# Performance work log

Measured on AMD Instinct MI355X. Metric: run time of the kernel, lower is better.

Reference implementation:

```python
import jax, jax.numpy as jnp
import numpy as np

N_NODES = 50000
N_EDGES = 1_600_000
IN_DIM, HID_DIM, OUT_DIM = 128, 128, 64


def setup_inputs() -> dict:
    key = jax.random.key(0)
    k_x, k_e, k_w1, k_b1, k_w2, k_b2 = jax.random.split(key, 6)
    x = jax.random.normal(k_x, (N_NODES, IN_DIM), dtype=jnp.float32)
    edge_index = jax.random.randint(k_e, (2, N_EDGES), 0, N_NODES)
    # Learned params (PyG GCNConv: linear weight + bias per layer)
    W1 = jax.random.normal(k_w1, (IN_DIM, HID_DIM), dtype=jnp.float32) * (1.0 / np.sqrt(IN_DIM))
    b1 = jax.random.normal(k_b1, (HID_DIM,), dtype=jnp.float32) * 0.02
    W2 = jax.random.normal(k_w2, (HID_DIM, OUT_DIM), dtype=jnp.float32) * (1.0 / np.sqrt(HID_DIM))
    b2 = jax.random.normal(k_b2, (OUT_DIM,), dtype=jnp.float32) * 0.02
    return {"x": x, "edge_index": edge_index, "W1": W1, "b1": b1, "W2": W2, "b2": b2}


def _gcn_conv(x, W, b, src, dst, norm, n):
    # x: [N, d_in]; transform first (d small), then gather-scale-scatter over edges.
    xw = x @ W                                   # [N, d_out]
    msg = xw[src] * norm[:, None]                # [E+N, d_out] gathered messages
    out = jax.ops.segment_sum(msg, dst, num_segments=n)
    return out + b


def reference(x, edge_index, W1, b1, W2, b2):
    n = x.shape[0]
    # GCN normalization with self-loops: A_hat = D^-1/2 (A + I) D^-1/2
    loop = jnp.arange(n, dtype=edge_index.dtype)
    src = jnp.concatenate([edge_index[0], loop])
    dst = jnp.concatenate([edge_index[1], loop])
    deg = jnp.zeros((n,), x.dtype).at[dst].add(1.0)
    dinv = jnp.where(deg > 0, jax.lax.rsqrt(deg), 0.0)
    norm = dinv[src] * dinv[dst]                 # [E+N]
    h = _gcn_conv(x, W1, b1, src, dst, norm, n)
    h = jax.nn.relu(h)
    # F.dropout(training=self.training): eval mode -> identity
    out = _gcn_conv(h, W2, b2, src, dst, norm, n)
    return out
```

## Files before the change

### kernel.cpp

```cpp
#include <hip/hip_runtime.h>
#include <cstddef>

#define MAXB 512
#define BSHIFT 7
#define ACHUNK 8192

__device__ inline unsigned pack_bf16x2(float a, float b) {
    unsigned ua = __float_as_uint(a), ub = __float_as_uint(b);
    ua = (ua + 0x7FFFu + ((ua >> 16) & 1u)) >> 16;
    ub = (ub + 0x7FFFu + ((ub >> 16) & 1u)) >> 16;
    return ua | (ub << 16);
}
__device__ inline float bf_lo(unsigned u) { return __uint_as_float(u << 16); }
__device__ inline float bf_hi(unsigned u) { return __uint_as_float(u & 0xFFFF0000u); }

__global__ __launch_bounds__(512) void k_zero512(int* __restrict__ p) {
    p[threadIdx.x] = 0;
}

__global__ __launch_bounds__(256) void k_histA(const int* __restrict__ dst, int* __restrict__ bcnt,
                                               int E, int nbuck) {
    __shared__ int hist[MAXB];
    const int tid = threadIdx.x;
    const int e0  = blockIdx.x * ACHUNK;
    const int e1  = min(e0 + ACHUNK, E);
    for (int i = tid; i < nbuck; i += 256) hist[i] = 0;
    __syncthreads();
    for (int e = e0 + tid; e < e1; e += 256)
        atomicAdd(&hist[dst[e] >> BSHIFT], 1);
    __syncthreads();
    for (int i = tid; i < nbuck; i += 256)
        if (hist[i]) atomicAdd(&bcnt[i], hist[i]);
}

__global__ __launch_bounds__(512) void k_bscan(const int* __restrict__ bcnt, int* __restrict__ bstart,
                                               int* __restrict__ bcur) {
    __shared__ int sh[512];
    const int t = threadIdx.x;
    int v = bcnt[t];
    sh[t] = v;
    __syncthreads();
    for (int d = 1; d < 512; d <<= 1) {
        int u = (t >= d) ? sh[t - d] : 0;
        __syncthreads();
        sh[t] += u;
        __syncthreads();
    }
    int ex = sh[t] - v;
    bstart[t] = ex;
    bcur[t]   = ex;
}

__global__ __launch_bounds__(256) void k_passA(const int* __restrict__ src, const int* __restrict__ dst,
                                               int* __restrict__ bcur, int2* __restrict__ tmp,
                                               int E, int nbuck) {
    __shared__ int hist[MAXB];
    __shared__ int gbase[MAXB];
    const int tid = threadIdx.x;
    const int e0  = blockIdx.x * ACHUNK;
    const int e1  = min(e0 + ACHUNK, E);
    for (int i = tid; i < nbuck; i += 256) hist[i] = 0;
    __syncthreads();
    for (int e = e0 + tid; e < e1; e += 256)
        atomicAdd(&hist[dst[e] >> BSHIFT], 1);
    __syncthreads();
    for (int i = tid; i < nbuck; i += 256) {
        int c = hist[i];
        gbase[i] = c ? atomicAdd(&bcur[i], c) : 0;
        hist[i] = 0;
    }
    __syncthreads();
    for (int e = e0 + tid; e < e1; e += 256) {
        int d = dst[e];
        int b = d >> BSHIFT;
        int slot = atomicAdd(&hist[b], 1);
        tmp[gbase[b] + slot] = make_int2(src[e], d);
    }
}

__global__ __launch_bounds__(256) void k_passB(const int2* __restrict__ tmp, const int* __restrict__ bstart,
                                               const int* __restrict__ bcnt, int* __restrict__ deg,
                                               float* __restrict__ dinv, int* __restrict__ off,
                                               int* __restrict__ esrc, int N) {
    __shared__ int cnt[1 << BSHIFT];
    __shared__ int loff[1 << BSHIFT];
    __shared__ int cur[1 << BSHIFT];
    const int b     = blockIdx.x;
    const int tid   = threadIdx.x;
    const int node0 = b << BSHIFT;
    const int base  = bstart[b];
    const int cntB  = bcnt[b];

    if (tid < 128) cnt[tid] = 0;
    __syncthreads();
    for (int i = tid; i < cntB; i += 256)
        atomicAdd(&cnt[tmp[base + i].y - node0], 1);
    __syncthreads();
    if (tid < 128) loff[tid] = cnt[tid];
    __syncthreads();
    for (int d = 1; d < 128; d <<= 1) {
        int u = (tid >= d && tid < 128) ? loff[tid - d] : 0;
        __syncthreads();
        if (tid < 128) loff[tid] += u;
        __syncthreads();
    }
    if (tid < 128) {
        int c  = cnt[tid];
        int ex = loff[tid] - c;
        cur[tid] = ex;
        if (node0 + tid < N) {
            deg [node0 + tid] = c + 1;
            dinv[node0 + tid] = rsqrtf((float)(c + 1));
            off [node0 + tid] = base + ex;
        }
    }
    __syncthreads();
    for (int i = tid; i < cntB; i += 256) {
        int2 ent = tmp[base + i];
        int  pos = atomicAdd(&cur[ent.y - node0], 1);
        esrc[base + pos] = ent.x;
    }
}

__global__ __launch_bounds__(256) void k_gemm1(const float* __restrict__ x, const float* __restrict__ W,
                                               unsigned* __restrict__ xwb, int M) {
    __shared__ float ws[128 * 128];
    __shared__ float xs[128][32];
    const int tid  = threadIdx.x;
    const int row0 = blockIdx.x * 32;

    for (int i = tid * 4; i < 128 * 128; i += 1024)
        *(float4*)&ws[i] = *(const float4*)&W[i];

    for (int i = tid; i < 32 * 32; i += 256) {
        int r  = i >> 5;
        int cc = (i & 31) << 2;
        float4 v = make_float4(0.f, 0.f, 0.f, 0.f);
        if (row0 + r < M) v = *(const float4*)&x[(size_t)(row0 + r) * 128 + cc];
        xs[cc + 0][r] = v.x; xs[cc + 1][r] = v.y; xs[cc + 2][r] = v.z; xs[cc + 3][r] = v.w;
    }
    __syncthreads();

    const int c0 = (tid & 31) << 2;
    const int r0 = (tid >> 5) << 2;
    float4 a0 = {0,0,0,0}, a1 = {0,0,0,0}, a2 = {0,0,0,0}, a3 = {0,0,0,0};
#pragma unroll 8
    for (int k = 0; k < 128; ++k) {
        float4 wv = *(const float4*)&ws[k * 128 + c0];
        float4 xv = *(const float4*)&xs[k][r0];
        a0.x += xv.x * wv.x; a0.y += xv.x * wv.y; a0.z += xv.x * wv.z; a0.w += xv.x * wv.w;
        a1.x += xv.y * wv.x; a1.y += xv.y * wv.y; a1.z += xv.y * wv.z; a1.w += xv.y * wv.w;
        a2.x += xv.z * wv.x; a2.y += xv.z * wv.y; a2.z += xv.z * wv.z; a2.w += xv.z * wv.w;
        a3.x += xv.w * wv.x; a3.y += xv.w * wv.y; a3.z += xv.w * wv.z; a3.w += xv.w * wv.w;
    }
    uint2* o = (uint2*)xwb;
    if (row0 + r0 + 0 < M) o[(size_t)(row0 + r0 + 0) * 32 + (c0 >> 2)] = make_uint2(pack_bf16x2(a0.x, a0.y), pack_bf16x2(a0.z, a0.w));
    if (row0 + r0 + 1 < M) o[(size_t)(row0 + r0 + 1) * 32 + (c0 >> 2)] = make_uint2(pack_bf16x2(a1.x, a1.y), pack_bf16x2(a1.z, a1.w));
    if (row0 + r0 + 2 < M) o[(size_t)(row0 + r0 + 2) * 32 + (c0 >> 2)] = make_uint2(pack_bf16x2(a2.x, a2.y), pack_bf16x2(a2.z, a2.w));
    if (row0 + r0 + 3 < M) o[(size_t)(row0 + r0 + 3) * 32 + (c0 >> 2)] = make_uint2(pack_bf16x2(a3.x, a3.y), pack_bf16x2(a3.z, a3.w));
}

__global__ __launch_bounds__(256) void k_gemm2(const float* __restrict__ h_in, const float* __restrict__ W,
                                               unsigned* __restrict__ hwb, int M) {
    __shared__ float ws[128 * 64];
    __shared__ float xs[128][32];
    const int tid  = threadIdx.x;
    const int row0 = blockIdx.x * 32;

    for (int i = tid * 4; i < 128 * 64; i += 1024)
        *(float4*)&ws[i] = *(const float4*)&W[i];

    for (int i = tid; i < 32 * 32; i += 256) {
        int r  = i >> 5;
        int cc = (i & 31) << 2;
        float4 v = make_float4(0.f, 0.f, 0.f, 0.f);
        if (row0 + r < M) {
            v = *(const float4*)&h_in[(size_t)(row0 + r) * 128 + cc];
            v.x = fmaxf(v.x, 0.f); v.y = fmaxf(v.y, 0.f);
            v.z = fmaxf(v.z, 0.f); v.w = fmaxf(v.w, 0.f);
        }
        xs[cc + 0][r] = v.x; xs[cc + 1][r] = v.y; xs[cc + 2][r] = v.z; xs[cc + 3][r] = v.w;
    }
    __syncthreads();

    const int c0 = (tid & 15) << 2;
    const int r0 = (tid >> 4) << 1;
    float4 a0 = {0,0,0,0}, a1 = {0,0,0,0};
#pragma unroll 8
    for (int k = 0; k < 128; ++k) {
        float4 wv = *(const float4*)&ws[k * 64 + c0];
        float2 xv = *(const float2*)&xs[k][r0];
        a0.x += xv.x * wv.x; a0.y += xv.x * wv.y; a0.z += xv.x * wv.z; a0.w += xv.x * wv.w;
        a1.x += xv.y * wv.x; a1.y += xv.y * wv.y; a1.z += xv.y * wv.z; a1.w += xv.y * wv.w;
    }
    uint2* o = (uint2*)hwb;
    if (row0 + r0 + 0 < M) o[(size_t)(row0 + r0 + 0) * 16 + (c0 >> 2)] = make_uint2(pack_bf16x2(a0.x, a0.y), pack_bf16x2(a0.z, a0.w));
    if (row0 + r0 + 1 < M) o[(size_t)(row0 + r0 + 1) * 16 + (c0 >> 2)] = make_uint2(pack_bf16x2(a1.x, a1.y), pack_bf16x2(a1.z, a1.w));
}

__global__ __launch_bounds__(256) void k_agg1(const uint2* __restrict__ xwb, const int* __restrict__ esrc,
                                              const int* __restrict__ off, const int* __restrict__ deg,
                                              const float* __restrict__ dinv, const float* __restrict__ b,
                                              float* __restrict__ out1, int N) {
    const int node = blockIdx.x * 4 + (threadIdx.x >> 6);
    if (node >= N) return;
    const int lane = threadIdx.x & 63;
    const int half = lane >> 5;
    const int lc   = lane & 31;
    const int c0   = lc << 2;

    const float di = dinv[node];
    float4 acc0 = {0,0,0,0}, acc1 = {0,0,0,0}, acc2 = {0,0,0,0}, acc3 = {0,0,0,0};
    if (half == 0) {
        float w0 = di * di;
        uint2  sv = xwb[(size_t)node * 32 + lc];
        float4 bb = *(const float4*)&b[c0];
        acc0.x = bb.x + bf_lo(sv.x) * w0; acc0.y = bb.y + bf_hi(sv.x) * w0;
        acc0.z = bb.z + bf_lo(sv.y) * w0; acc0.w = bb.w + bf_hi(sv.y) * w0;
    }

    const int base = off[node];
    const int cnt  = deg[node] - 1;
    for (int p0 = 0; p0 < cnt; p0 += 64) {
        int   es = 0;
        float ew = 0.f;
        if (p0 + lane < cnt) {
            es = esrc[base + p0 + lane];
            ew = dinv[es] * di;
        }
        const int take = min(64, cnt - p0);
        int j = 0;
        for (; j + 8 <= take; j += 8) {
            int i0 = j + half, i1 = j + 2 + half, i2 = j + 4 + half, i3 = j + 6 + half;
            int   s0 = __shfl(es, i0); float w0f = __shfl(ew, i0);
            int   s1 = __shfl(es, i1); float w1f = __shfl(ew, i1);
            int   s2 = __shfl(es, i2); float w2f = __shfl(ew, i2);
            int   s3 = __shfl(es, i3); float w3f = __shfl(ew, i3);
            uint2 v0 = xwb[(size_t)s0 * 32 + lc];
            uint2 v1 = xwb[(size_t)s1 * 32 + lc];
            uint2 v2 = xwb[(size_t)s2 * 32 + lc];
            uint2 v3 = xwb[(size_t)s3 * 32 + lc];
            acc0.x += bf_lo(v0.x) * w0f; acc0.y += bf_hi(v0.x) * w0f;
            acc0.z += bf_lo(v0.y) * w0f; acc0.w += bf_hi(v0.y) * w0f;
            acc1.x += bf_lo(v1.x) * w1f; acc1.y += bf_hi(v1.x) * w1f;
            acc1.z += bf_lo(v1.y) * w1f; acc1.w += bf_hi(v1.y) * w1f;
            acc2.x += bf_lo(v2.x) * w2f; acc2.y += bf_hi(v2.x) * w2f;
            acc2.z += bf_lo(v2.y) * w2f; acc2.w += bf_hi(v2.y) * w2f;
            acc3.x += bf_lo(v3.x) * w3f; acc3.y += bf_hi(v3.x) * w3f;
            acc3.z += bf_lo(v3.y) * w3f; acc3.w += bf_hi(v3.y) * w3f;
        }
        for (; j < take; j += 2) {
            int i0 = j + half;
            int   s0 = __shfl(es, i0); float w0f = __shfl(ew, i0);
            uint2 v0 = xwb[(size_t)s0 * 32 + lc];
            acc0.x += bf_lo(v0.x) * w0f; acc0.y += bf_hi(v0.x) * w0f;
            acc0.z += bf_lo(v0.y) * w0f; acc0.w += bf_hi(v0.y) * w0f;
        }
    }
    acc0.x += acc1.x + acc2.x + acc3.x;
    acc0.y += acc1.y + acc2.y + acc3.y;
    acc0.z += acc1.z + acc2.z + acc3.z;
    acc0.w += acc1.w + acc2.w + acc3.w;
    acc0.x += __shfl_xor(acc0.x, 32);
    acc0.y += __shfl_xor(acc0.y, 32);
    acc0.z += __shfl_xor(acc0.z, 32);
    acc0.w += __shfl_xor(acc0.w, 32);
    if (half == 0) *(float4*)&out1[(size_t)node * 128 + c0] = acc0;
}

__global__ __launch_bounds__(256) void k_agg2(const uint2* __restrict__ hwb, const int* __restrict__ esrc,
                                              const int* __restrict__ off, const int* __restrict__ deg,
                                              const float* __restrict__ dinv, const float* __restrict__ b,
                                              float* __restrict__ out, int N) {
    const int node = blockIdx.x * 4 + (threadIdx.x >> 6);
    if (node >= N) return;
    const int lane = threadIdx.x & 63;
    const int grp  = lane >> 4;
    const int lc   = lane & 15;
    const int c0   = lc << 2;

    const float di = dinv[node];
    float4 acc0 = {0,0,0,0}, acc1 = {0,0,0,0}, acc2 = {0,0,0,0}, acc3 = {0,0,0,0};
    if (grp == 0) {
        float w0 = di * di;
        uint2  sv = hwb[(size_t)node * 16 + lc];
        float4 bb = *(const float4*)&b[c0];
        acc0.x = bb.x + bf_lo(sv.x) * w0; acc0.y = bb.y + bf_hi(sv.x) * w0;
        acc0.z = bb.z + bf_lo(sv.y) * w0; acc0.w = bb.w + bf_hi(sv.y) * w0;
    }

    const int base = off[node];
    const int cnt  = deg[node] - 1;
    for (int p0 = 0; p0 < cnt; p0 += 64) {
        int   es = 0;
        float ew = 0.f;
        if (p0 + lane < cnt) {
            es = esrc[base + p0 + lane];
            ew = dinv[es] * di;
        }
        const int take = min(64, cnt - p0);
        int j = 0;
        for (; j + 16 <= take; j += 16) {
            int i0 = j + grp, i1 = j + 4 + grp, i2 = j + 8 + grp, i3 = j + 12 + grp;
            int   s0 = __shfl(es, i0); float w0f = __shfl(ew, i0);
            int   s1 = __shfl(es, i1); float w1f = __shfl(ew, i1);
            int   s2 = __shfl(es, i2); float w2f = __shfl(ew, i2);
            int   s3 = __shfl(es, i3); float w3f = __shfl(ew, i3);
            uint2 v0 = hwb[(size_t)s0 * 16 + lc];
            uint2 v1 = hwb[(size_t)s1 * 16 + lc];
            uint2 v2 = hwb[(size_t)s2 * 16 + lc];
            uint2 v3 = hwb[(size_t)s3 * 16 + lc];
            acc0.x += bf_lo(v0.x) * w0f; acc0.y += bf_hi(v0.x) * w0f;
            acc0.z += bf_lo(v0.y) * w0f; acc0.w += bf_hi(v0.y) * w0f;
            acc1.x += bf_lo(v1.x) * w1f; acc1.y += bf_hi(v1.x) * w1f;
            acc1.z += bf_lo(v1.y) * w1f; acc1.w += bf_hi(v1.y) * w1f;
            acc2.x += bf_lo(v2.x) * w2f; acc2.y += bf_hi(v2.x) * w2f;
            acc2.z += bf_lo(v2.y) * w2f; acc2.w += bf_hi(v2.y) * w2f;
            acc3.x += bf_lo(v3.x) * w3f; acc3.y += bf_hi(v3.x) * w3f;
            acc3.z += bf_lo(v3.y) * w3f; acc3.w += bf_hi(v3.y) * w3f;
        }
        for (; j < take; j += 4) {
            int i0 = j + grp;
            int   s0 = __shfl(es, i0); float w0f = __shfl(ew, i0);
            uint2 v0 = hwb[(size_t)s0 * 16 + lc];
            acc0.x += bf_lo(v0.x) * w0f; acc0.y += bf_hi(v0.x) * w0f;
            acc0.z += bf_lo(v0.y) * w0f; acc0.w += bf_hi(v0.y) * w0f;
        }
    }
    acc0.x += acc1.x + acc2.x + acc3.x;
    acc0.y += acc1.y + acc2.y + acc3.y;
    acc0.z += acc1.z + acc2.z + acc3.z;
    acc0.w += acc1.w + acc2.w + acc3.w;
    acc0.x += __shfl_xor(acc0.x, 16); acc0.y += __shfl_xor(acc0.y, 16);
    acc0.z += __shfl_xor(acc0.z, 16); acc0.w += __shfl_xor(acc0.w, 16);
    acc0.x += __shfl_xor(acc0.x, 32); acc0.y += __shfl_xor(acc0.y, 32);
    acc0.z += __shfl_xor(acc0.z, 32); acc0.w += __shfl_xor(acc0.w, 32);
    if (lane < 16) *(float4*)&out[(size_t)node * 64 + c0] = acc0;
}

extern "C" void kernel_launch(void* const* d_in, const int* in_sizes, int n_in,
                              void* d_out, int out_size, void* d_ws, size_t ws_size,
                              hipStream_t stream) {
    const float* x  = (const float*)d_in[0];
    const int*   ei = (const int*)  d_in[1];
    const float* W1 = (const float*)d_in[2];
    const float* b1 = (const float*)d_in[3];
    const float* W2 = (const float*)d_in[4];
    const float* b2 = (const float*)d_in[5];
    float* out = (float*)d_out;

    const int N = in_sizes[0] / 128;
    const int E = in_sizes[1] / 2;
    const int* src = ei;
    const int* dst = ei + E;
    const int NBUCK = (N + 127) / 128;
    const int NA    = (E + ACHUNK - 1) / ACHUNK;

    char* w = (char*)d_ws;
    int*      deg     = (int*)w;              w += (size_t)N * 4;
    float*    dinv    = (float*)w;            w += (size_t)N * 4;
    int*      off     = (int*)w;              w += (size_t)N * 4;
    int*      bstart  = (int*)w;              w += 512 * 4;
    int*      bcnt    = (int*)w;              w += 512 * 4;
    int*      bcur    = (int*)w;              w += 512 * 4;
    int*      esrc    = (int*)w;              w += (size_t)E * 4;
    unsigned* xwb     = (unsigned*)w;         w += (size_t)N * 128 * 2;
    float*    out1    = (float*)w;            w += (size_t)N * 128 * 4;
    unsigned* hwb     = (unsigned*)w;
    int2*     tmp     = (int2*)out1;

    k_zero512 <<<1, 512, 0, stream>>>(bcnt);
    k_histA   <<<NA, 256, 0, stream>>>(dst, bcnt, E, NBUCK);
    k_bscan   <<<1, 512, 0, stream>>>(bcnt, bstart, bcur);
    k_passA   <<<NA, 256, 0, stream>>>(src, dst, bcur, tmp, E, NBUCK);
    k_passB   <<<NBUCK, 256, 0, stream>>>(tmp, bstart, bcnt, deg, dinv, off, esrc, N);

    k_gemm1 <<<(N + 31) / 32, 256, 0, stream>>>(x, W1, xwb, N);
    k_agg1  <<<(N + 3) / 4, 256, 0, stream>>>((const uint2*)xwb, esrc, off, deg, dinv, b1, out1, N);

    k_gemm2 <<<(N + 31) / 32, 256, 0, stream>>>(out1, W2, hwb, N);
    k_agg2  <<<(N + 3) / 4, 256, 0, stream>>>((const uint2*)hwb, esrc, off, deg, dinv, b2, out, N);
}
```

Before: 248.7 us.

## Bin edges by source chunk and process 8 nodes per wave for gather locality

```diff
diff --git a/kernel.cpp b/kernel.cpp
--- a/kernel.cpp
+++ b/kernel.cpp
@@ -4,6 +4,9 @@
 #define MAXB 512
 #define BSHIFT 7
 #define ACHUNK 8192
+#define CSHIFT 13
+#define NCH 7
+#define NPW 8
 
 __device__ inline unsigned pack_bf16x2(float a, float b) {
     unsigned ua = __float_as_uint(a), ub = __float_as_uint(b);
@@ -79,24 +82,34 @@
 }
 
 __global__ __launch_bounds__(256) void k_passB(const int2* __restrict__ tmp, const int* __restrict__ bstart,
-                                               const int* __restrict__ bcnt, int* __restrict__ deg,
-                                               float* __restrict__ dinv, int* __restrict__ off,
-                                               int* __restrict__ esrc, int N) {
-    __shared__ int cnt[1 << BSHIFT];
-    __shared__ int loff[1 << BSHIFT];
-    __shared__ int cur[1 << BSHIFT];
+                                               const int* __restrict__ bcnt, float* __restrict__ dinv,
+                                               int* __restrict__ coff, int* __restrict__ esrc, int N) {
+    __shared__ int cnt2[128 * NCH];
+    __shared__ int cur2[128 * NCH];
+    __shared__ int tot[128];
+    __shared__ int loff[128];
     const int b     = blockIdx.x;
     const int tid   = threadIdx.x;
     const int node0 = b << BSHIFT;
     const int base  = bstart[b];
     const int cntB  = bcnt[b];
 
-    if (tid < 128) cnt[tid] = 0;
-    __syncthreads();
-    for (int i = tid; i < cntB; i += 256)
-        atomicAdd(&cnt[tmp[base + i].y - node0], 1);
-    __syncthreads();
-    if (tid < 128) loff[tid] = cnt[tid];
+    for (int i = tid; i < 128 * NCH; i += 256) cnt2[i] = 0;
+    __syncthreads();
+    for (int i = tid; i < cntB; i += 256) {
+        int2 ent = tmp[base + i];
+        int  nl  = ent.y - node0;
+        int  c   = min(ent.x >> CSHIFT, NCH - 1);
+        atomicAdd(&cnt2[nl * NCH + c], 1);
+    }
+    __syncthreads();
+    if (tid < 128) {
+        int t = 0;
+#pragma unroll
+        for (int c = 0; c < NCH; ++c) t += cnt2[tid * NCH + c];
+        tot[tid] = t;
+        loff[tid] = t;
+    }
     __syncthreads();
     for (int d = 1; d < 128; d <<= 1) {
         int u = (tid >= d && tid < 128) ? loff[tid - d] : 0;
@@ -105,20 +118,27 @@
         __syncthreads();
     }
     if (tid < 128) {
-        int c  = cnt[tid];
-        int ex = loff[tid] - c;
-        cur[tid] = ex;
-        if (node0 + tid < N) {
-            deg [node0 + tid] = c + 1;
-            dinv[node0 + tid] = rsqrtf((float)(c + 1));
-            off [node0 + tid] = base + ex;
+        int t  = tot[tid];
+        int p  = base + loff[tid] - t;
+        int gn = node0 + tid;
+        if (gn < N) {
+            dinv[gn] = rsqrtf((float)(t + 1));
+#pragma unroll
+            for (int c = 0; c < NCH; ++c) {
+                coff[(size_t)gn * 8 + c] = p;
+                cur2[tid * NCH + c] = p;
+                p += cnt2[tid * NCH + c];
+            }
+            coff[(size_t)gn * 8 + 7] = p;
         }
     }
     __syncthreads();
     for (int i = tid; i < cntB; i += 256) {
         int2 ent = tmp[base + i];
-        int  pos = atomicAdd(&cur[ent.y - node0], 1);
-        esrc[base + pos] = ent.x;
+        int  nl  = ent.y - node0;
+        int  c   = min(ent.x >> CSHIFT, NCH - 1);
+        int  pos = atomicAdd(&cur2[nl * NCH + c], 1);
+        esrc[pos] = ent.x;
     }
 }
 
@@ -199,143 +219,181 @@
 }
 
 __global__ __launch_bounds__(256) void k_agg1(const uint2* __restrict__ xwb, const int* __restrict__ esrc,
-                                              const int* __restrict__ off, const int* __restrict__ deg,
-                                              const float* __restrict__ dinv, const float* __restrict__ b,
-                                              float* __restrict__ out1, int N) {
-    const int node = blockIdx.x * 4 + (threadIdx.x >> 6);
-    if (node >= N) return;
+                                              const int* __restrict__ coff, const float* __restrict__ dinv,
+                                              const float* __restrict__ b, float* __restrict__ out1, int N) {
+    const int wid   = blockIdx.x * 4 + (threadIdx.x >> 6);
+    const int node0 = wid * NPW;
+    if (node0 >= N) return;
     const int lane = threadIdx.x & 63;
     const int half = lane >> 5;
     const int lc   = lane & 31;
     const int c0   = lc << 2;
-
-    const float di = dinv[node];
-    float4 acc0 = {0,0,0,0}, acc1 = {0,0,0,0}, acc2 = {0,0,0,0}, acc3 = {0,0,0,0};
-    if (half == 0) {
-        float w0 = di * di;
-        uint2  sv = xwb[(size_t)node * 32 + lc];
-        float4 bb = *(const float4*)&b[c0];
-        acc0.x = bb.x + bf_lo(sv.x) * w0; acc0.y = bb.y + bf_hi(sv.x) * w0;
-        acc0.z = bb.z + bf_lo(sv.y) * w0; acc0.w = bb.w + bf_hi(sv.y) * w0;
-    }
-
-    const int base = off[node];
-    const int cnt  = deg[node] - 1;
-    for (int p0 = 0; p0 < cnt; p0 += 64) {
-        int   es = 0;
-        float ew = 0.f;
-        if (p0 + lane < cnt) {
-            es = esrc[base + p0 + lane];
-            ew = dinv[es] * di;
-        }
-        const int take = min(64, cnt - p0);
-        int j = 0;
-        for (; j + 8 <= take; j += 8) {
-            int i0 = j + half, i1 = j + 2 + half, i2 = j + 4 + half, i3 = j + 6 + half;
-            int   s0 = __shfl(es, i0); float w0f = __shfl(ew, i0);
-            int   s1 = __shfl(es, i1); float w1f = __shfl(ew, i1);
-            int   s2 = __shfl(es, i2); float w2f = __shfl(ew, i2);
-            int   s3 = __shfl(es, i3); float w3f = __shfl(ew, i3);
-            uint2 v0 = xwb[(size_t)s0 * 32 + lc];
-            uint2 v1 = xwb[(size_t)s1 * 32 + lc];
-            uint2 v2 = xwb[(size_t)s2 * 32 + lc];
-            uint2 v3 = xwb[(size_t)s3 * 32 + lc];
-            acc0.x += bf_lo(v0.x) * w0f; acc0.y += bf_hi(v0.x) * w0f;
-            acc0.z += bf_lo(v0.y) * w0f; acc0.w += bf_hi(v0.y) * w0f;
-            acc1.x += bf_lo(v1.x) * w1f; acc1.y += bf_hi(v1.x) * w1f;
-            acc1.z += bf_lo(v1.y) * w1f; acc1.w += bf_hi(v1.y) * w1f;
-            acc2.x += bf_lo(v2.x) * w2f; acc2.y += bf_hi(v2.x) * w2f;
-            acc2.z += bf_lo(v2.y) * w2f; acc2.w += bf_hi(v2.y) * w2f;
-            acc3.x += bf_lo(v3.x) * w3f; acc3.y += bf_hi(v3.x) * w3f;
-            acc3.z += bf_lo(v3.y) * w3f; acc3.w += bf_hi(v3.y) * w3f;
-        }
-        for (; j < take; j += 2) {
-            int i0 = j + half;
-            int   s0 = __shfl(es, i0); float w0f = __shfl(ew, i0);
-            uint2 v0 = xwb[(size_t)s0 * 32 + lc];
-            acc0.x += bf_lo(v0.x) * w0f; acc0.y += bf_hi(v0.x) * w0f;
-            acc0.z += bf_lo(v0.y) * w0f; acc0.w += bf_hi(v0.y) * w0f;
-        }
-    }
-    acc0.x += acc1.x + acc2.x + acc3.x;
-    acc0.y += acc1.y + acc2.y + acc3.y;
-    acc0.z += acc1.z + acc2.z + acc3.z;
-    acc0.w += acc1.w + acc2.w + acc3.w;
-    acc0.x += __shfl_xor(acc0.x, 32);
-    acc0.y += __shfl_xor(acc0.y, 32);
-    acc0.z += __shfl_xor(acc0.z, 32);
-    acc0.w += __shfl_xor(acc0.w, 32);
-    if (half == 0) *(float4*)&out1[(size_t)node * 128 + c0] = acc0;
+    const float4 bb = *(const float4*)&b[c0];
+
+    float4 acc[NPW];
+    float  dis[NPW];
+#pragma unroll
+    for (int i = 0; i < NPW; ++i) {
+        acc[i] = make_float4(0.f, 0.f, 0.f, 0.f);
+        dis[i] = 0.f;
+        int node = node0 + i;
+        if (node < N) {
+            float di = dinv[node];
+            dis[i] = di;
+            if (half == 0) {
+                float w0 = di * di;
+                uint2 sv = xwb[(size_t)node * 32 + lc];
+                acc[i].x = bb.x + bf_lo(sv.x) * w0; acc[i].y = bb.y + bf_hi(sv.x) * w0;
+                acc[i].z = bb.z + bf_lo(sv.y) * w0; acc[i].w = bb.w + bf_hi(sv.y) * w0;
+            }
+        }
+    }
+
+    for (int c = 0; c < NCH; ++c) {
+#pragma unroll
+        for (int i = 0; i < NPW; ++i) {
+            int node = node0 + i;
+            if (node < N) {
+                const float di = dis[i];
+                const int s = coff[(size_t)node * 8 + c];
+                const int e = coff[(size_t)node * 8 + c + 1];
+                for (int p0 = s; p0 < e; p0 += 64) {
+                    int   es = 0;
+                    float ew = 0.f;
+                    if (p0 + lane < e) { es = esrc[p0 + lane]; ew = dinv[es] * di; }
+                    const int take = min(64, e - p0);
+                    int j = 0;
+                    for (; j + 8 <= take; j += 8) {
+                        int i0 = j + half, i1 = j + 2 + half, i2 = j + 4 + half, i3 = j + 6 + half;
+                        int   s0 = __shfl(es, i0); float w0f = __shfl(ew, i0);
+                        int   s1 = __shfl(es, i1); float w1f = __shfl(ew, i1);
+                        int   s2 = __shfl(es, i2); float w2f = __shfl(ew, i2);
+                        int   s3 = __shfl(es, i3); float w3f = __shfl(ew, i3);
+                        uint2 v0 = xwb[(size_t)s0 * 32 + lc];
+                        uint2 v1 = xwb[(size_t)s1 * 32 + lc];
+                        uint2 v2 = xwb[(size_t)s2 * 32 + lc];
+                        uint2 v3 = xwb[(size_t)s3 * 32 + lc];
+                        acc[i].x += bf_lo(v0.x) * w0f; acc[i].y += bf_hi(v0.x) * w0f;
+                        acc[i].z += bf_lo(v0.y) * w0f; acc[i].w += bf_hi(v0.y) * w0f;
+                        acc[i].x += bf_lo(v1.x) * w1f; acc[i].y += bf_hi(v1.x) * w1f;
+                        acc[i].z += bf_lo(v1.y) * w1f; acc[i].w += bf_hi(v1.y) * w1f;
+                        acc[i].x += bf_lo(v2.x) * w2f; acc[i].y += bf_hi(v2.x) * w2f;
+                        acc[i].z += bf_lo(v2.y) * w2f; acc[i].w += bf_hi(v2.y) * w2f;
+                        acc[i].x += bf_lo(v3.x) * w3f; acc[i].y += bf_hi(v3.x) * w3f;
+                        acc[i].z += bf_lo(v3.y) * w3f; acc[i].w += bf_hi(v3.y) * w3f;
+                    }
+                    for (; j < take; j += 2) {
+                        int i0 = j + half;
+                        int   s0 = __shfl(es, i0); float w0f = __shfl(ew, i0);
+                        uint2 v0 = xwb[(size_t)s0 * 32 + lc];
+                        acc[i].x += bf_lo(v0.x) * w0f; acc[i].y += bf_hi(v0.x) * w0f;
+                        acc[i].z += bf_lo(v0.y) * w0f; acc[i].w += bf_hi(v0.y) * w0f;
+                    }
+                }
+            }
+        }
+    }
+#pragma unroll
+    for (int i = 0; i < NPW; ++i) {
+        int node = node0 + i;
+        if (node < N) {
+            float4 a = acc[i];
+            a.x += __shfl_xor(a.x, 32); a.y += __shfl_xor(a.y, 32);
+            a.z += __shfl_xor(a.z, 32); a.w += __shfl_xor(a.w, 32);
+            if (half == 0) *(float4*)&out1[(size_t)node * 128 + c0] = a;
+        }
+    }
 }
 
 __global__ __launch_bounds__(256) void k_agg2(const uint2* __restrict__ hwb, const int* __restrict__ esrc,
-                                              const int* __restrict__ off, const int* __restrict__ deg,
-                                              const float* __restrict__ dinv, const float* __restrict__ b,
-                                              float* __restrict__ out, int N) {
-    const int node = blockIdx.x * 4 + (threadIdx.x >> 6);
-    if (node >= N) return;
+                                              const int* __restrict__ coff, const float* __restrict__ dinv,
+                                              const float* __restrict__ b, float* __restrict__ out, int N) {
+    const int wid   = blockIdx.x * 4 + (threadIdx.x >> 6);
+    const int node0 = wid * NPW;
+    if (node0 >= N) return;
     const int lane = threadIdx.x & 63;
     const int grp  = lane >> 4;
     const int lc   = lane & 15;
     const int c0   = lc << 2;
-
-    const float di = dinv[node];
-    float4 acc0 = {0,0,0,0}, acc1 = {0,0,0,0}, acc2 = {0,0,0,0}, acc3 = {0,0,0,0};
-    if (grp == 0) {
-        float w0 = di * di;
-        uint2  sv = hwb[(size_t)node * 16 + lc];
-        float4 bb = *(const float4*)&b[c0];
-        acc0.x = bb.x + bf_lo(sv.x) * w0; acc0.y = bb.y + bf_hi(sv.x) * w0;
-        acc0.z = bb.z + bf_lo(sv.y) * w0; acc0.w = bb.w + bf_hi(sv.y) * w0;
-    }
-
-    const int base = off[node];
-    const int cnt  = deg[node] - 1;
-    for (int p0 = 0; p0 < cnt; p0 += 64) {
-        int   es = 0;
-        float ew = 0.f;
-        if (p0 + lane < cnt) {
-            es = esrc[base + p0 + lane];
-            ew = dinv[es] * di;
-        }
-        const int take = min(64, cnt - p0);
-        int j = 0;
-        for (; j + 16 <= take; j += 16) {
-            int i0 = j + grp, i1 = j + 4 + grp, i2 = j + 8 + grp, i3 = j + 12 + grp;
-            int   s0 = __shfl(es, i0); float w0f = __shfl(ew, i0);
-            int   s1 = __shfl(es, i1); float w1f = __shfl(ew, i1);
-            int   s2 = __shfl(es, i2); float w2f = __shfl(ew, i2);
-            int   s3 = __shfl(es, i3); float w3f = __shfl(ew, i3);
-            uint2 v0 = hwb[(size_t)s0 * 16 + lc];
-            uint2 v1 = hwb[(size_t)s1 * 16 + lc];
-            uint2 v2 = hwb[(size_t)s2 * 16 + lc];
-            uint2 v3 = hwb[(size_t)s3 * 16 + lc];
-            acc0.x += bf_lo(v0.x) * w0f; acc0.y += bf_hi(v0.x) * w0f;
-            acc0.z += bf_lo(v0.y) * w0f; acc0.w += bf_hi(v0.y) * w0f;
-            acc1.x += bf_lo(v1.x) * w1f; acc1.y += bf_hi(v1.x) * w1f;
-            acc1.z += bf_lo(v1.y) * w1f; acc1.w += bf_hi(v1.y) * w1f;
-            acc2.x += bf_lo(v2.x) * w2f; acc2.y += bf_hi(v2.x) * w2f;
-            acc2.z += bf_lo(v2.y) * w2f; acc2.w += bf_hi(v2.y) * w2f;
-            acc3.x += bf_lo(v3.x) * w3f; acc3.y += bf_hi(v3.x) * w3f;
-            acc3.z += bf_lo(v3.y) * w3f; acc3.w += bf_hi(v3.y) * w3f;
-        }
-        for (; j < take; j += 4) {
-            int i0 = j + grp;
-            int   s0 = __shfl(es, i0); float w0f = __shfl(ew, i0);
-            uint2 v0 = hwb[(size_t)s0 * 16 + lc];
-            acc0.x += bf_lo(v0.x) * w0f; acc0.y += bf_hi(v0.x) * w0f;
-            acc0.z += bf_lo(v0.y) * w0f; acc0.w += bf_hi(v0.y) * w0f;
-        }
-    }
-    acc0.x += acc1.x + acc2.x + acc3.x;
-    acc0.y += acc1.y + acc2.y + acc3.y;
-    acc0.z += acc1.z + acc2.z + acc3.z;
-    acc0.w += acc1.w + acc2.w + acc3.w;
-    acc0.x += __shfl_xor(acc0.x, 16); acc0.y += __shfl_xor(acc0.y, 16);
-    acc0.z += __shfl_xor(acc0.z, 16); acc0.w += __shfl_xor(acc0.w, 16);
-    acc0.x += __shfl_xor(acc0.x, 32); acc0.y += __shfl_xor(acc0.y, 32);
-    acc0.z += __shfl_xor(acc0.z, 32); acc0.w += __shfl_xor(acc0.w, 32);
-    if (lane < 16) *(float4*)&out[(size_t)node * 64 + c0] = acc0;
+    const float4 bb = *(const float4*)&b[c0];
+
+    float4 acc[NPW];
+    float  dis[NPW];
+#pragma unroll
+    for (int i = 0; i < NPW; ++i) {
+        acc[i] = make_float4(0.f, 0.f, 0.f, 0.f);
+        dis[i] = 0.f;
+        int node = node0 + i;
+        if (node < N) {
+            float di = dinv[node];
+            dis[i] = di;
+            if (grp == 0) {
+                float w0 = di * di;
+                uint2 sv = hwb[(size_t)node * 16 + lc];
+                acc[i].x = bb.x + bf_lo(sv.x) * w0; acc[i].y = bb.y + bf_hi(sv.x) * w0;
+                acc[i].z = bb.z + bf_lo(sv.y) * w0; acc[i].w = bb.w + bf_hi(sv.y) * w0;
+            }
+        }
+    }
+
+    for (int c2 = 0; c2 < 4; ++c2) {
+        const int si = 2 * c2;
+        const int ei = (si + 2 < 7) ? (si + 2) : 7;
+#pragma unroll
+        for (int i = 0; i < NPW; ++i) {
+            int node = node0 + i;
+            if (node < N) {
+                const float di = dis[i];
+                const int s = coff[(size_t)node * 8 + si];
+                const int e = coff[(size_t)node * 8 + ei];
+                for (int p0 = s; p0 < e; p0 += 64) {
+                    int   es = 0;
+                    float ew = 0.f;
+                    if (p0 + lane < e) { es = esrc[p0 + lane]; ew = dinv[es] * di; }
+                    const int take = min(64, e - p0);
+                    int j = 0;
+                    for (; j + 16 <= take; j += 16) {
+                        int i0 = j + grp, i1 = j + 4 + grp, i2 = j + 8 + grp, i3 = j + 12 + grp;
+                        int   s0 = __shfl(es, i0); float w0f = __shfl(ew, i0);
+                        int   s1 = __shfl(es, i1); float w1f = __shfl(ew, i1);
+                        int   s2 = __shfl(es, i2); float w2f = __shfl(ew, i2);
+                        int   s3 = __shfl(es, i3); float w3f = __shfl(ew, i3);
+                        uint2 v0 = hwb[(size_t)s0 * 16 + lc];
+                        uint2 v1 = hwb[(size_t)s1 * 16 + lc];
+                        uint2 v2 = hwb[(size_t)s2 * 16 + lc];
+                        uint2 v3 = hwb[(size_t)s3 * 16 + lc];
+                        acc[i].x += bf_lo(v0.x) * w0f; acc[i].y += bf_hi(v0.x) * w0f;
+                        acc[i].z += bf_lo(v0.y) * w0f; acc[i].w += bf_hi(v0.y) * w0f;
+                        acc[i].x += bf_lo(v1.x) * w1f; acc[i].y += bf_hi(v1.x) * w1f;
+                        acc[i].z += bf_lo(v1.y) * w1f; acc[i].w += bf_hi(v1.y) * w1f;
+                        acc[i].x += bf_lo(v2.x) * w2f; acc[i].y += bf_hi(v2.x) * w2f;
+                        acc[i].z += bf_lo(v2.y) * w2f; acc[i].w += bf_hi(v2.y) * w2f;
+                        acc[i].x += bf_lo(v3.x) * w3f; acc[i].y += bf_hi(v3.x) * w3f;
+                        acc[i].z += bf_lo(v3.y) * w3f; acc[i].w += bf_hi(v3.y) * w3f;
+                    }
+                    for (; j < take; j += 4) {
+                        int i0 = j + grp;
+                        int   s0 = __shfl(es, i0); float w0f = __shfl(ew, i0);
+                        uint2 v0 = hwb[(size_t)s0 * 16 + lc];
+                        acc[i].x += bf_lo(v0.x) * w0f; acc[i].y += bf_hi(v0.x) * w0f;
+                        acc[i].z += bf_lo(v0.y) * w0f; acc[i].w += bf_hi(v0.y) * w0f;
+                    }
+                }
+            }
+        }
+    }
+#pragma unroll
+    for (int i = 0; i < NPW; ++i) {
+        int node = node0 + i;
+        if (node < N) {
+            float4 a = acc[i];
+            a.x += __shfl_xor(a.x, 16); a.y += __shfl_xor(a.y, 16);
+            a.z += __shfl_xor(a.z, 16); a.w += __shfl_xor(a.w, 16);
+            a.x += __shfl_xor(a.x, 32); a.y += __shfl_xor(a.y, 32);
+            a.z += __shfl_xor(a.z, 32); a.w += __shfl_xor(a.w, 32);
+            if (lane < 16) *(float4*)&out[(size_t)node * 64 + c0] = a;
+        }
+    }
 }
 
 extern "C" void kernel_launch(void* const* d_in, const int* in_sizes, int n_in,
@@ -355,11 +413,11 @@
     const int* dst = ei + E;
     const int NBUCK = (N + 127) / 128;
     const int NA    = (E + ACHUNK - 1) / ACHUNK;
+    const int NAGG  = ((N + NPW - 1) / NPW + 3) / 4;
 
     char* w = (char*)d_ws;
-    int*      deg     = (int*)w;              w += (size_t)N * 4;
     float*    dinv    = (float*)w;            w += (size_t)N * 4;
-    int*      off     = (int*)w;              w += (size_t)N * 4;
+    int*      coff    = (int*)w;              w += (size_t)N * 8 * 4;
     int*      bstart  = (int*)w;              w += 512 * 4;
     int*      bcnt    = (int*)w;              w += 512 * 4;
     int*      bcur    = (int*)w;              w += 512 * 4;
@@ -373,11 +431,11 @@
     k_histA   <<<NA, 256, 0, stream>>>(dst, bcnt, E, NBUCK);
     k_bscan   <<<1, 512, 0, stream>>>(bcnt, bstart, bcur);
     k_passA   <<<NA, 256, 0, stream>>>(src, dst, bcur, tmp, E, NBUCK);
-    k_passB   <<<NBUCK, 256, 0, stream>>>(tmp, bstart, bcnt, deg, dinv, off, esrc, N);
+    k_passB   <<<NBUCK, 256, 0, stream>>>(tmp, bstart, bcnt, dinv, coff, esrc, N);
 
     k_gemm1 <<<(N + 31) / 32, 256, 0, stream>>>(x, W1, xwb, N);
-    k_agg1  <<<(N + 3) / 4, 256, 0, stream>>>((const uint2*)xwb, esrc, off, deg, dinv, b1, out1, N);
+    k_agg1  <<<NAGG, 256, 0, stream>>>((const uint2*)xwb, esrc, coff, dinv, b1, out1, N);
 
     k_gemm2 <<<(N + 31) / 32, 256, 0, stream>>>(out1, W2, hwb, N);
-    k_agg2  <<<(N + 3) / 4, 256, 0, stream>>>((const uint2*)hwb, esrc, off, deg, dinv, b2, out, N);
-}
+    k_agg2  <<<NAGG, 256, 0, stream>>>((const uint2*)hwb, esrc, coff, dinv, b2, out, N);
+}
```

Measured after the change: 422.0 us. +69.7%, slower.
